# Performance work log

Hardware: AMD Instinct MI355X
Metric: run time of the kernel (lower is better)

## Reference

```python
import jax, jax.numpy as jnp
import numpy as np

HEAD_DIM = 64
FEAT_H, FEAT_W = 64, 64
ROPE_THETA = 10000.0


def axial_rope_cache(dim, height, width, theta):
    # Matches compute_axial_rope_cache: interleaved cos/sin of shape [H*W, dim]
    theta_dim = (dim // 2) // 2
    freqs = 1.0 / theta ** (jnp.arange(theta_dim, dtype=jnp.float32) * 2.0 / theta_dim)
    t_x = jnp.tile(jnp.arange(width, dtype=jnp.float32)[None, :], (height, 1)).reshape(-1)
    t_y = jnp.tile(jnp.arange(height, dtype=jnp.float32)[:, None], (1, width)).reshape(-1)
    theta_all = jnp.concatenate([jnp.outer(t_x, freqs), jnp.outer(t_y, freqs)], axis=-1)
    cos = jnp.repeat(jnp.cos(theta_all), 2, axis=-1)  # [H*W, dim]
    sin = jnp.repeat(jnp.sin(theta_all), 2, axis=-1)
    return cos, sin


def apply_rope(x, cos, sin):
    # x: [B, H, N, D]; cos/sin: [N, D]
    x1 = x[..., 0::2]
    x2 = x[..., 1::2]
    rot = jnp.stack([-x2, x1], axis=-1).reshape(x.shape)
    return x * cos[None, None] + rot * sin[None, None]


def setup_inputs() -> dict:
    key = jax.random.key(0)
    ks = jax.random.split(key, 11)
    B, Nq, Nk, E, KVD, ID = 1, 4096, 8192, 256, 64, 256
    s_e = 1.0 / np.sqrt(E)
    s_kv = 1.0 / np.sqrt(KVD)
    s_i = 1.0 / np.sqrt(ID)
    return {
        "query": jax.random.normal(ks[0], (B, Nq, E), jnp.float32),
        "key": jax.random.normal(ks[1], (B, Nk, KVD), jnp.float32),
        "value": jax.random.normal(ks[2], (B, Nk, KVD), jnp.float32),
        "Wq": jax.random.normal(ks[3], (E, ID), jnp.float32) * s_e,
        "bq": jnp.zeros((ID,), jnp.float32),
        "Wk": jax.random.normal(ks[4], (KVD, ID), jnp.float32) * s_kv,
        "bk": jnp.zeros((ID,), jnp.float32),
        "Wv": jax.random.normal(ks[5], (KVD, ID), jnp.float32) * s_kv,
        "bv": jnp.zeros((ID,), jnp.float32),
        "Wo": jax.random.normal(ks[6], (ID, E), jnp.float32) * s_i,
        "bo": jnp.zeros((E,), jnp.float32),
        "num_k_exclude_rope": 0,
    }


def reference(query, key, value, Wq, bq, Wk, bk, Wv, bv, Wo, bo, num_k_exclude_rope):
    B, Nq, _ = query.shape
    Nk = key.shape[1]
    H, D = 4, HEAD_DIM

    def split_heads(x):
        b, n, c = x.shape
        return x.reshape(b, n, H, c // H).transpose(0, 2, 1, 3)

    q = split_heads(query @ Wq + bq)  # [B,H,Nq,D]
    k = split_heads(key @ Wk + bk)    # [B,H,Nk,D]
    v = split_heads(value @ Wv + bv)

    cos, sin = axial_rope_cache(D, FEAT_H, FEAT_W, ROPE_THETA)  # [4096, D]
    q = apply_rope(q, cos, sin)

    num_k_rope = Nk - num_k_exclude_rope
    k_spatial = k[:, :, :num_k_rope, :]
    k_other = k[:, :, num_k_rope:, :]
    repeats = num_k_rope // cos.shape[0]  # rope_k_repeat=True
    cos_k = jnp.tile(cos, (repeats, 1))
    sin_k = jnp.tile(sin, (repeats, 1))
    k_spatial = apply_rope(k_spatial, cos_k, sin_k)
    k = jnp.concatenate([k_spatial, k_other], axis=2)

    q = q / jnp.sqrt(jnp.asarray(D, q.dtype))
    scores = jnp.einsum("bhqd,bhkd->bhqk", q, k)
    attn = jax.nn.softmax(scores, axis=-1)
    out = jnp.einsum("bhqk,bhkd->bhqd", attn, v)
    out = out.transpose(0, 2, 1, 3).reshape(B, Nq, H * D)
    return out @ Wo + bo
```

## Files before the change

### kernel.cpp

```cpp
#include <hip/hip_runtime.h>
#include <hip/hip_bf16.h>

#define NQ 4096
#define NK 8192
#define NSPLIT 8
#define KSPAN (NK / NSPLIT)
#define BK 64

#define QSCALE 0.1803368801111204f

typedef short v8s __attribute__((ext_vector_type(8)));
typedef float v4f __attribute__((ext_vector_type(4)));

static __device__ __forceinline__ unsigned short f2bf(float f) {
    unsigned int u = __float_as_uint(f);
    u = (u + 0x7FFFu + ((u >> 16) & 1u)) >> 16;
    return (unsigned short)u;
}
static __device__ __forceinline__ float bf2f(unsigned short h) {
    return __uint_as_float(((unsigned int)h) << 16);
}
static __device__ __forceinline__ unsigned int pkbf(float a, float b) {
    union { __hip_bfloat162 h; unsigned int u; } cv;
    cv.h = __float22bfloat162_rn(make_float2(a, b));
    return cv.u;
}
static __device__ __forceinline__ void split8(const float* a, v8s& hi, v8s& lo) {
#pragma unroll
    for (int j = 0; j < 8; ++j) {
        unsigned short h = f2bf(a[j]);
        hi[j] = (short)h;
        lo[j] = (short)f2bf(a[j] - bf2f(h));
    }
}
static __device__ __forceinline__ void wload(const unsigned short* __restrict__ H,
                                             const unsigned short* __restrict__ L,
                                             int k0, int col, v8s& wh, v8s& wl) {
    const size_t f = (size_t)((k0 >> 3) * 256 + col) * 8;
    wh = *(const v8s*)(H + f);
    wl = *(const v8s*)(L + f);
}
static __device__ __forceinline__ void dma16(const unsigned short* g, unsigned short* l) {
    __builtin_amdgcn_global_load_lds(
        (const __attribute__((address_space(1))) unsigned int*)(const void*)g,
        (__attribute__((address_space(3))) unsigned int*)(void*)l, 16, 0, 0);
}

__global__ __launch_bounds__(256) void prep_kernel(
    const float* __restrict__ Wq, const float* __restrict__ Wk,
    const float* __restrict__ Wv, const float* __restrict__ Wo,
    unsigned short* __restrict__ WqH, unsigned short* __restrict__ WqL,
    unsigned short* __restrict__ WkH, unsigned short* __restrict__ WkL,
    unsigned short* __restrict__ WvH, unsigned short* __restrict__ WvL,
    unsigned short* __restrict__ WoH, unsigned short* __restrict__ WoL)
{
    const int tid = blockIdx.x * 256 + threadIdx.x;
    const float* W;
    unsigned short *H, *L;
    int f;
    if (tid < 8192)        { W = Wq; H = WqH; L = WqL; f = tid; }
    else if (tid < 10240)  { W = Wk; H = WkH; L = WkL; f = tid - 8192; }
    else if (tid < 12288)  { W = Wv; H = WvH; L = WvL; f = tid - 10240; }
    else                   { W = Wo; H = WoH; L = WoL; f = tid - 12288; }
    const int col = f & 255, k0 = (f >> 8) << 3;
    float wv[8];
#pragma unroll
    for (int j = 0; j < 8; ++j) wv[j] = W[(size_t)(k0 + j) * 256 + col];
    v8s hi, lo;
    split8(wv, hi, lo);
    *(v8s*)(H + (size_t)f * 8) = hi;
    *(v8s*)(L + (size_t)f * 8) = lo;
}

__global__ __launch_bounds__(256) void qkv_kernel(
    const float* __restrict__ query, const float* __restrict__ key,
    const float* __restrict__ value,
    const unsigned short* __restrict__ WqH, const unsigned short* __restrict__ WqL,
    const unsigned short* __restrict__ WkH, const unsigned short* __restrict__ WkL,
    const unsigned short* __restrict__ WvH, const unsigned short* __restrict__ WvL,
    const float* __restrict__ bq, const float* __restrict__ bk,
    const float* __restrict__ bv,
    unsigned short* __restrict__ Qb, unsigned short* __restrict__ Kb,
    unsigned short* __restrict__ Vt, const int* __restrict__ nexp)
{
    const int b = blockIdx.x;
    const int t = threadIdx.x, w = t >> 6, lane = t & 63;
    const int quad = lane >> 4, l16 = lane & 15;
    const int colbase = w * 64;

    if (b < 256) {
        const int n0 = b * 16;
        v4f acc[4];
#pragma unroll
        for (int ct = 0; ct < 4; ++ct) {
            const float bb = bq[colbase + ct * 16 + l16];
            acc[ct] = v4f{bb, bb, bb, bb};
        }
        const float* arow = query + (size_t)(n0 + l16) * 256 + quad * 8;
#pragma unroll
        for (int k0 = 0; k0 < 256; k0 += 32) {
            float av[8];
            *(float4*)av = *(const float4*)(arow + k0);
            *(float4*)(av + 4) = *(const float4*)(arow + k0 + 4);
            v8s ah, al;
            split8(av, ah, al);
#pragma unroll
            for (int ct = 0; ct < 4; ++ct) {
                v8s wh, wl;
                wload(WqH, WqL, k0 + quad * 8, colbase + ct * 16 + l16, wh, wl);
                acc[ct] = __builtin_amdgcn_mfma_f32_16x16x32_bf16(al, wh, acc[ct], 0, 0, 0);
                acc[ct] = __builtin_amdgcn_mfma_f32_16x16x32_bf16(ah, wl, acc[ct], 0, 0, 0);
                acc[ct] = __builtin_amdgcn_mfma_f32_16x16x32_bf16(ah, wh, acc[ct], 0, 0, 0);
            }
        }
#pragma unroll
        for (int ct = 0; ct < 4; ++ct) {
            const int d = ct * 16 + l16;
            const int j = d >> 1;
            const float freq = exp2f(-(float)(j & 15) * 1.66096404744368f);
            const bool isx = (j < 16), odd = (d & 1);
#pragma unroll
            for (int r = 0; r < 4; ++r) {
                const int p = n0 + quad * 4 + r;
                const float tpos = isx ? (float)(p & 63) : (float)(p >> 6);
                float sn, cs;
                __sincosf(tpos * freq, &sn, &cs);
                const float x = acc[ct][r];
                const float xp = __shfl_xor(x, 1, 64);
                const float y = odd ? fmaf(x, cs, xp * sn) : fmaf(x, cs, -xp * sn);
                Qb[((size_t)(w * NQ + p) << 6) + d] = f2bf(y * QSCALE);
            }
        }
    } else {
        const bool isK = (b < 768);
        const int n0 = (isK ? (b - 256) : (b - 768)) * 16;
        const float* X = isK ? key : value;
        const unsigned short* WH = isK ? WkH : WvH;
        const unsigned short* WL = isK ? WkL : WvL;
        const float* bias = isK ? bk : bv;
        v4f acc[4];
#pragma unroll
        for (int ct = 0; ct < 4; ++ct) {
            const float bb = bias[colbase + ct * 16 + l16];
            acc[ct] = v4f{bb, bb, bb, bb};
        }
        const float* arow = X + (size_t)(n0 + l16) * 64 + quad * 8;
#pragma unroll
        for (int k0 = 0; k0 < 64; k0 += 32) {
            float av[8];
            *(float4*)av = *(const float4*)(arow + k0);
            *(float4*)(av + 4) = *(const float4*)(arow + k0 + 4);
            v8s ah, al;
            split8(av, ah, al);
#pragma unroll
            for (int ct = 0; ct < 4; ++ct) {
                v8s wh, wl;
                wload(WH, WL, k0 + quad * 8, colbase + ct * 16 + l16, wh, wl);
                acc[ct] = __builtin_amdgcn_mfma_f32_16x16x32_bf16(al, wh, acc[ct], 0, 0, 0);
                acc[ct] = __builtin_amdgcn_mfma_f32_16x16x32_bf16(ah, wl, acc[ct], 0, 0, 0);
                acc[ct] = __builtin_amdgcn_mfma_f32_16x16x32_bf16(ah, wh, acc[ct], 0, 0, 0);
            }
        }
        if (isK) {
            const int nro = NK - *nexp;
#pragma unroll
            for (int ct = 0; ct < 4; ++ct) {
                const int d = ct * 16 + l16;
                const int j = d >> 1;
                const float freq = exp2f(-(float)(j & 15) * 1.66096404744368f);
                const bool isx = (j < 16), odd = (d & 1);
#pragma unroll
                for (int r = 0; r < 4; ++r) {
                    const int p = n0 + quad * 4 + r;
                    const int pc = p & 4095;
                    const float tpos = isx ? (float)(pc & 63) : (float)(pc >> 6);
                    float sn, cs;
                    __sincosf(tpos * freq, &sn, &cs);
                    const float x = acc[ct][r];
                    const float xp = __shfl_xor(x, 1, 64);
                    float y = odd ? fmaf(x, cs, xp * sn) : fmaf(x, cs, -xp * sn);
                    y = (p < nro) ? y : x;
                    Kb[((size_t)(w * NK + p) << 6) + d] = f2bf(y);
                }
            }
        } else {
#pragma unroll
            for (int ct = 0; ct < 4; ++ct) {
                const int col = colbase + ct * 16 + l16;
                uint2 u = make_uint2(pkbf(acc[ct][0], acc[ct][1]),
                                     pkbf(acc[ct][2], acc[ct][3]));
                *(uint2*)(Vt + (size_t)col * NK + n0 + quad * 4) = u;
            }
        }
    }
}

__global__ __launch_bounds__(256) void attn_kernel(
    const unsigned short* __restrict__ Qb, const unsigned short* __restrict__ Kb,
    const unsigned short* __restrict__ Vt, unsigned short* __restrict__ Opart,
    float* __restrict__ Lbuf)
{
    __shared__ alignas(16) unsigned short Kl[64 * 64];
    __shared__ alignas(16) unsigned short Vl[64 * 64];

    const int blk = blockIdx.x;
    const int s = blk & 7, h = (blk >> 3) & 3, qt = blk >> 5;
    const int t = threadIdx.x;
    const int w = t >> 6, lane = t & 63;
    const int quad = lane >> 4, l16 = lane & 15;

    const int q0 = qt * 128 + w * 32;
    v8s qf[2][2];
#pragma unroll
    for (int g = 0; g < 2; ++g) {
        const unsigned short* qr = Qb + ((size_t)(h * NQ + q0 + g * 16 + l16) << 6) + quad * 8;
        qf[g][0] = *(const v8s*)qr;
        qf[g][1] = *(const v8s*)(qr + 32);
    }

    v4f O[4][2];
#pragma unroll
    for (int dt = 0; dt < 4; ++dt)
#pragma unroll
        for (int g = 0; g < 2; ++g) O[dt][g] = v4f{0.f, 0.f, 0.f, 0.f};
    float psum[2] = {0.f, 0.f};

    const unsigned short* Kbase = Kb + (((size_t)h * NK + s * KSPAN) << 6);
    const unsigned short* Vbase = Vt + (size_t)(h * 64) * NK + s * KSPAN;

    const int srow = lane >> 3;
    const int schunk = (lane & 7) ^ srow;
    const int c0off = ((quad ^ (l16 & 7)) * 8);
    const int c1off = c0off ^ 32;
    int voff[2][2];
#pragma unroll
    for (int tv = 0; tv < 2; ++tv)
#pragma unroll
        for (int h2 = 0; h2 < 2; ++h2)
            voff[tv][h2] = (((4 * tv + 2 * h2 + (quad >> 1)) ^ (l16 & 7)) << 3) + 4 * (quad & 1);

    for (int k0 = 0; k0 < KSPAN; k0 += BK) {
        __syncthreads();
#pragma unroll
        for (int half = 0; half < 2; ++half) {
            const int r0 = w * 16 + half * 8;
            dma16(Kbase + ((size_t)(k0 + r0 + srow) << 6) + schunk * 8, &Kl[r0 * 64]);
            dma16(Vbase + (size_t)(r0 + srow) * NK + k0 + schunk * 8, &Vl[r0 * 64]);
        }
        __syncthreads();

        v8s pf[2][2];
#pragma unroll
        for (int tt = 0; tt < 4; ++tt) {
            const unsigned short* kr = &Kl[(tt * 16 + l16) * 64];
            const v8s kf0 = *(const v8s*)(kr + c0off);
            const v8s kf1 = *(const v8s*)(kr + c1off);
#pragma unroll
            for (int g = 0; g < 2; ++g) {
                v4f a = v4f{0.f, 0.f, 0.f, 0.f};
                a = __builtin_amdgcn_mfma_f32_16x16x32_bf16(kf0, qf[g][0], a, 0, 0, 0);
                a = __builtin_amdgcn_mfma_f32_16x16x32_bf16(kf1, qf[g][1], a, 0, 0, 0);
                const float e0 = __builtin_amdgcn_exp2f(a[0]);
                const float e1 = __builtin_amdgcn_exp2f(a[1]);
                const float e2 = __builtin_amdgcn_exp2f(a[2]);
                const float e3 = __builtin_amdgcn_exp2f(a[3]);
                psum[g] += (e0 + e1) + (e2 + e3);
                unsigned int* pp = (unsigned int*)&pf[g][tt >> 1];
                pp[(tt & 1) * 2 + 0] = pkbf(e0, e1);
                pp[(tt & 1) * 2 + 1] = pkbf(e2, e3);
            }
        }

#pragma unroll
        for (int dt = 0; dt < 4; ++dt) {
            const unsigned short* vr = &Vl[(dt * 16 + l16) * 64];
#pragma unroll
            for (int tv = 0; tv < 2; ++tv) {
                union { v8s s; uint2 u[2]; } vv;
                vv.u[0] = *(const uint2*)(vr + voff[tv][0]);
                vv.u[1] = *(const uint2*)(vr + voff[tv][1]);
#pragma unroll
                for (int g = 0; g < 2; ++g)
                    O[dt][g] = __builtin_amdgcn_mfma_f32_16x16x32_bf16(vv.s, pf[g][tv], O[dt][g], 0, 0, 0);
            }
        }
    }

#pragma unroll
    for (int g = 0; g < 2; ++g) {
        float p = psum[g];
        p += __shfl_xor(p, 16, 64);
        p += __shfl_xor(p, 32, 64);
        psum[g] = p;
    }
    unsigned short* Ob = Opart + (size_t)blk * 8192;
#pragma unroll
    for (int g = 0; g < 2; ++g) {
        const int row = w * 32 + g * 16 + l16;
#pragma unroll
        for (int dt = 0; dt < 4; ++dt) {
            uint2 u = make_uint2(pkbf(O[dt][g][0], O[dt][g][1]),
                                 pkbf(O[dt][g][2], O[dt][g][3]));
            *(uint2*)(Ob + row * 64 + dt * 16 + quad * 4) = u;
        }
        if (quad == 0) Lbuf[blk * 128 + row] = psum[g];
    }
}

__global__ __launch_bounds__(256) void oreduce_kernel(
    const unsigned short* __restrict__ Opart, const float* __restrict__ Lbuf,
    unsigned short* __restrict__ OredH, unsigned short* __restrict__ OredL)
{
    const int tid = blockIdx.x * 256 + threadIdx.x;
    const int e0 = tid << 3;
    const int r = e0 >> 8, d0 = e0 & 255;
    const int h = d0 >> 6;
    const int qt = r >> 7, rr = r & 127;
    const int base = qt * 32 + h * 8;
    const unsigned short* op = Opart + (size_t)base * 8192 + rr * 64 + (d0 & 63);
    float lsum = 0.f;
    float o[8] = {0.f, 0.f, 0.f, 0.f, 0.f, 0.f, 0.f, 0.f};
#pragma unroll
    for (int s = 0; s < NSPLIT; ++s) {
        lsum += Lbuf[(base + s) * 128 + rr];
        v8s a = *(const v8s*)(op + (size_t)s * 8192);
#pragma unroll
        for (int j = 0; j < 8; ++j) o[j] += bf2f((unsigned short)a[j]);
    }
    const float inv = 1.f / lsum;
#pragma unroll
    for (int j = 0; j < 8; ++j) o[j] *= inv;
    v8s hi, lo;
    split8(o, hi, lo);
    *(v8s*)(OredH + (size_t)r * 256 + d0) = hi;
    *(v8s*)(OredL + (size_t)r * 256 + d0) = lo;
}

__global__ __launch_bounds__(256) void oproj_kernel(
    const unsigned short* __restrict__ OredH, const unsigned short* __restrict__ OredL,
    const unsigned short* __restrict__ WoH, const unsigned short* __restrict__ WoL,
    const float* __restrict__ bo, float* __restrict__ out)
{
    const int t = threadIdx.x, w = t >> 6, lane = t & 63;
    const int quad = lane >> 4, l16 = lane & 15;
    const int n0 = (blockIdx.x >> 2) * 16;
    const int col = (blockIdx.x & 3) * 64 + w * 16 + l16;
    const float bb = bo[col];
    v4f acc = v4f{bb, bb, bb, bb};
    const unsigned short* ah_row = OredH + (size_t)(n0 + l16) * 256 + quad * 8;
    const unsigned short* al_row = OredL + (size_t)(n0 + l16) * 256 + quad * 8;
#pragma unroll
    for (int k0 = 0; k0 < 256; k0 += 32) {
        v8s ah = *(const v8s*)(ah_row + k0);
        v8s al = *(const v8s*)(al_row + k0);
        v8s wh, wl;
        wload(WoH, WoL, k0 + quad * 8, col, wh, wl);
        acc = __builtin_amdgcn_mfma_f32_16x16x32_bf16(al, wh, acc, 0, 0, 0);
        acc = __builtin_amdgcn_mfma_f32_16x16x32_bf16(ah, wl, acc, 0, 0, 0);
        acc = __builtin_amdgcn_mfma_f32_16x16x32_bf16(ah, wh, acc, 0, 0, 0);
    }
#pragma unroll
    for (int r = 0; r < 4; ++r)
        out[(size_t)(n0 + quad * 4 + r) * 256 + col] = acc[r];
}

extern "C" void kernel_launch(void* const* d_in, const int* in_sizes, int n_in,
                              void* d_out, int out_size, void* d_ws, size_t ws_size,
                              hipStream_t stream) {
    const float* query = (const float*)d_in[0];
    const float* key   = (const float*)d_in[1];
    const float* value = (const float*)d_in[2];
    const float* Wq    = (const float*)d_in[3];
    const float* bq    = (const float*)d_in[4];
    const float* Wk    = (const float*)d_in[5];
    const float* bk    = (const float*)d_in[6];
    const float* Wv    = (const float*)d_in[7];
    const float* bv    = (const float*)d_in[8];
    const float* Wo    = (const float*)d_in[9];
    const float* bo    = (const float*)d_in[10];
    const int*   nex   = (const int*)d_in[11];

    char* ws = (char*)d_ws;
    const size_t MB = 1024 * 1024;
    unsigned short* Qb    = (unsigned short*)(ws);
    unsigned short* Kb    = (unsigned short*)(ws + 2 * MB);
    unsigned short* Vt    = (unsigned short*)(ws + 6 * MB);
    unsigned short* Opart = (unsigned short*)(ws + 10 * MB);
    float* Lbuf           = (float*)(ws + 26 * MB);
    unsigned short* OredH = (unsigned short*)(ws + 26 * MB + 512 * 1024);
    unsigned short* OredL = (unsigned short*)(ws + 28 * MB + 512 * 1024);
    unsigned short* Wpl   = (unsigned short*)(ws + 30 * MB + 512 * 1024);
    unsigned short* WqH = Wpl;
    unsigned short* WqL = Wpl + 65536;
    unsigned short* WkH = Wpl + 131072;
    unsigned short* WkL = Wpl + 147456;
    unsigned short* WvH = Wpl + 163840;
    unsigned short* WvL = Wpl + 180224;
    unsigned short* WoH = Wpl + 196608;
    unsigned short* WoL = Wpl + 262144;
    float* out = (float*)d_out;

    prep_kernel<<<80, 256, 0, stream>>>(Wq, Wk, Wv, Wo,
                                        WqH, WqL, WkH, WkL, WvH, WvL, WoH, WoL);
    qkv_kernel<<<1280, 256, 0, stream>>>(query, key, value,
                                         WqH, WqL, WkH, WkL, WvH, WvL,
                                         bq, bk, bv, Qb, Kb, Vt, nex);
    attn_kernel<<<1024, 256, 0, stream>>>(Qb, Kb, Vt, Opart, Lbuf);
    oreduce_kernel<<<512, 256, 0, stream>>>(Opart, Lbuf, OredH, OredL);
    oproj_kernel<<<1024, 256, 0, stream>>>(OredH, OredL, WoH, WoL, bo, out);
}
```

Before: 158.9 us.

## Double-buffer K/V LDS tiles to overlap DMA prefetch with MFMA compute

Splits the shared K and V tiles into two buffers. The next tile's direct-to-LDS loads are issued before computing on the current tile, which hides global-load latency behind the QK^T/exp/PV MFMA work. The loop keeps one barrier per iteration instead of two, and raises wave priority around the compute section. The cost is doubled LDS use (32KB per block), which may reduce occupancy, plus a correctness dependence on the vmcnt wait covering the DMA writes before the buffer swap.

```diff
diff --git a/kernel.cpp b/kernel.cpp
--- a/kernel.cpp
+++ b/kernel.cpp
@@ -200,8 +200,8 @@
     const unsigned short* __restrict__ Vt, unsigned short* __restrict__ Opart,
     float* __restrict__ Lbuf)
 {
-    __shared__ alignas(16) unsigned short Kl[64 * 64];
-    __shared__ alignas(16) unsigned short Vl[64 * 64];
+    __shared__ alignas(16) unsigned short Kl[2][64 * 64];
+    __shared__ alignas(16) unsigned short Vl[2][64 * 64];
 
     const int blk = blockIdx.x;
     const int s = blk & 7, h = (blk >> 3) & 3, qt = blk >> 5;
@@ -239,20 +239,39 @@
         for (int h2 = 0; h2 < 2; ++h2)
             voff[tv][h2] = (((4 * tv + 2 * h2 + (quad >> 1)) ^ (l16 & 7)) << 3) + 4 * (quad & 1);
 
-    for (int k0 = 0; k0 < KSPAN; k0 += BK) {
-        __syncthreads();
-#pragma unroll
-        for (int half = 0; half < 2; ++half) {
-            const int r0 = w * 16 + half * 8;
-            dma16(Kbase + ((size_t)(k0 + r0 + srow) << 6) + schunk * 8, &Kl[r0 * 64]);
-            dma16(Vbase + (size_t)(r0 + srow) * NK + k0 + schunk * 8, &Vl[r0 * 64]);
-        }
-        __syncthreads();
+    const int NT = KSPAN / BK;
+
+#pragma unroll
+    for (int half = 0; half < 2; ++half) {
+        const int r0 = w * 16 + half * 8;
+        dma16(Kbase + ((size_t)(r0 + srow) << 6) + schunk * 8, &Kl[0][r0 * 64]);
+        dma16(Vbase + (size_t)(r0 + srow) * NK + schunk * 8, &Vl[0][r0 * 64]);
+    }
+    asm volatile("s_waitcnt vmcnt(0)" ::: "memory");
+    __builtin_amdgcn_s_barrier();
+    __builtin_amdgcn_sched_barrier(0);
+
+    for (int it = 0; it < NT; ++it) {
+        const int cur = it & 1;
+        const unsigned short* Klc = &Kl[cur][0];
+        const unsigned short* Vlc = &Vl[cur][0];
+
+        if (it + 1 < NT) {
+            const int k1 = (it + 1) * BK;
+#pragma unroll
+            for (int half = 0; half < 2; ++half) {
+                const int r0 = w * 16 + half * 8;
+                dma16(Kbase + ((size_t)(k1 + r0 + srow) << 6) + schunk * 8, &Kl[cur ^ 1][r0 * 64]);
+                dma16(Vbase + (size_t)(r0 + srow) * NK + k1 + schunk * 8, &Vl[cur ^ 1][r0 * 64]);
+            }
+        }
+        __builtin_amdgcn_sched_barrier(0);
+        __builtin_amdgcn_s_setprio(1);
 
         v8s pf[2][2];
 #pragma unroll
         for (int tt = 0; tt < 4; ++tt) {
-            const unsigned short* kr = &Kl[(tt * 16 + l16) * 64];
+            const unsigned short* kr = &Klc[(tt * 16 + l16) * 64];
             const v8s kf0 = *(const v8s*)(kr + c0off);
             const v8s kf1 = *(const v8s*)(kr + c1off);
 #pragma unroll
@@ -273,7 +292,7 @@
 
 #pragma unroll
         for (int dt = 0; dt < 4; ++dt) {
-            const unsigned short* vr = &Vl[(dt * 16 + l16) * 64];
+            const unsigned short* vr = &Vlc[(dt * 16 + l16) * 64];
 #pragma unroll
             for (int tv = 0; tv < 2; ++tv) {
                 union { v8s s; uint2 u[2]; } vv;
@@ -284,6 +303,11 @@
                     O[dt][g] = __builtin_amdgcn_mfma_f32_16x16x32_bf16(vv.s, pf[g][tv], O[dt][g], 0, 0, 0);
             }
         }
+        __builtin_amdgcn_s_setprio(0);
+
+        asm volatile("s_waitcnt vmcnt(0)" ::: "memory");
+        __builtin_amdgcn_s_barrier();
+        __builtin_amdgcn_sched_barrier(0);
     }
 
 #pragma unroll
```

After: 161.6 us. About the same (+1.7%).
